# Kernel tuning notes

Hardware: AMD Instinct MI355X
Metric: run time of the kernel (lower is better)

The kernel has to match this reference:

```python
import jax, jax.numpy as jnp
import numpy as np

S, B, D, H, L = 512, 64, 1024, 1024, 2


def setup_inputs() -> dict:
    key = jax.random.key(0)
    ks = jax.random.split(key, 10)
    stdv = 1.0 / np.sqrt(H)
    u = lambda k, shp: jax.random.uniform(k, shp, jnp.float32, -stdv, stdv)
    return {
        "x": jax.random.normal(ks[0], (S, B, D), jnp.float32),
        "hx": jnp.zeros((L, B, H), jnp.float32),
        "w_ih_0": u(ks[1], (3 * H, D)),
        "w_hh_0": u(ks[2], (3 * H, H)),
        "b_ih_0": u(ks[3], (3 * H,)),
        "b_hh_0": u(ks[4], (3 * H,)),
        "w_ih_1": u(ks[5], (3 * H, H)),
        "w_hh_1": u(ks[6], (3 * H, H)),
        "b_ih_1": u(ks[7], (3 * H,)),
        "b_hh_1": u(ks[8], (3 * H,)),
    }


def _gru_layer(x, h0, w_ih, w_hh, b_ih, b_hh):
    # Input-to-hidden projection for the whole sequence in one GEMM (same math,
    # x_t does not depend on the recurrence).  (S,B,3H)
    x_lin = jnp.einsum('sbd,gd->sbg', x, w_ih) + b_ih

    def step(h, xl):
        x_r, x_z, x_n = jnp.split(xl, 3, axis=-1)
        h_lin = h @ w_hh.T + b_hh  # (B,3H)
        h_r, h_z, h_n = jnp.split(h_lin, 3, axis=-1)
        r = jax.nn.sigmoid(x_r + h_r)
        z = jax.nn.sigmoid(x_z + h_z)
        n = jnp.tanh(x_n + r * h_n)
        h_new = (1.0 - z) * n + z * h
        return h_new, h_new

    h_last, ys = jax.lax.scan(step, h0, x_lin)
    return ys, h_last


def reference(x, hx, w_ih_0, w_hh_0, b_ih_0, b_hh_0,
              w_ih_1, w_hh_1, b_ih_1, b_hh_1):
    out0, h_f0 = _gru_layer(x, hx[0], w_ih_0, w_hh_0, b_ih_0, b_hh_0)
    out1, h_f1 = _gru_layer(out0, hx[1], w_ih_1, w_hh_1, b_ih_1, b_hh_1)
    hidden = jnp.stack([h_f0, h_f1], axis=0)  # (L,B,H)
    return out1, hidden
```

## Files before the change

### kernel.cpp

```cpp
#include <hip/hip_runtime.h>
#include <stdint.h>


#define SLEN 512
#define HB   65536
#define G3   3072
#define XLSLOT (64 * 64 * 48)

typedef __attribute__((ext_vector_type(8))) short bf16x8;
typedef __attribute__((ext_vector_type(4))) float f32x4;
typedef __attribute__((ext_vector_type(8))) uint16_t u16x8;

__device__ __forceinline__ uint16_t f32_to_bf16(float f) {
  uint32_t u = __float_as_uint(f);
  uint32_t r = u + 0x7FFFu + ((u >> 16) & 1u);
  return (uint16_t)(r >> 16);
}
__device__ __forceinline__ float sigmoid_fast(float x) { return 1.0f / (1.0f + __expf(-x)); }
__device__ __forceinline__ float tanh_fast(float x) { return 1.0f - 2.0f / (1.0f + __expf(2.0f * x)); }
__device__ __forceinline__ void async_cp16(const void* g, void* l) {
  __builtin_amdgcn_global_load_lds((const __attribute__((address_space(1))) void*)g,
                                   (__attribute__((address_space(3))) void*)l, 16, 0, 0);
}
__device__ __forceinline__ void st_u16_llc(uint16_t* p, uint16_t v) {
  __hip_atomic_store(p, v, __ATOMIC_RELAXED, __HIP_MEMORY_SCOPE_AGENT);
}
__device__ __forceinline__ void st_f32_llc(float* p, float v) {
  __hip_atomic_store(p, v, __ATOMIC_RELAXED, __HIP_MEMORY_SCOPE_AGENT);
}
__device__ __forceinline__ void drain_vmem() {
  asm volatile("s_waitcnt vmcnt(0)" ::: "memory");
}
__device__ __forceinline__ int ld_flag(const int* p) {
  return __hip_atomic_load(p, __ATOMIC_RELAXED, __HIP_MEMORY_SCOPE_AGENT);
}
__device__ __forceinline__ void st_flag(int* p, int v) {
  __hip_atomic_store(p, v, __ATOMIC_RELAXED, __HIP_MEMORY_SCOPE_AGENT);
}


__global__ __launch_bounds__(256) void convert_x(const float* __restrict__ src,
                                                 uint16_t* __restrict__ dst) {
  size_t i = ((size_t)blockIdx.x * 256 + threadIdx.x) * 8;
  const float4* s = (const float4*)(src + i);
  float4 a = s[0], b = s[1];
  u16x8 v;
  v[0] = f32_to_bf16(a.x); v[1] = f32_to_bf16(a.y);
  v[2] = f32_to_bf16(a.z); v[3] = f32_to_bf16(a.w);
  v[4] = f32_to_bf16(b.x); v[5] = f32_to_bf16(b.y);
  v[6] = f32_to_bf16(b.z); v[7] = f32_to_bf16(b.w);
  *(u16x8*)(dst + i) = v;
}

__global__ __launch_bounds__(256) void pack_w(const float* __restrict__ src,
                                              uint16_t* __restrict__ dst) {
  int tid = blockIdx.x * 256 + threadIdx.x;
  int tile = tid >> 11, rem = tid & 2047, ks = rem >> 6, lane = rem & 63;
  int row = tile * 16 + (lane & 15);
  int k0 = ks * 32 + (lane >> 4) * 8;
  const float* s = src + (size_t)row * 1024 + k0;
  u16x8 v;
#pragma unroll
  for (int j = 0; j < 8; ++j) v[j] = f32_to_bf16(s[j]);
  *(u16x8*)(dst + (size_t)tid * 8) = v;
}

__global__ __launch_bounds__(256) void init_state(const float* __restrict__ hx,
                                                  uint16_t* __restrict__ h0b,
                                                  uint16_t* __restrict__ h1b,
                                                  int* __restrict__ flags) {
  int i = blockIdx.x * 256 + threadIdx.x;
  h0b[i] = f32_to_bf16(hx[i]);
  h1b[i] = f32_to_bf16(hx[HB + i]);
  if (blockIdx.x < 16) flags[blockIdx.x * 256 + threadIdx.x] = 0;
}

__device__ __forceinline__ void poll_wait(const int* p0, int t0,
                                          const int* pa, int ta,
                                          const int* pb, int tb, int lane) {
  const int BIG = 0x7fffffff;
  int v0 = (t0 > 0) ? ld_flag(p0) : BIG;
  int va = (ta > 0) ? ld_flag(pa + lane * 16) : BIG;
  int vb = (tb > 0) ? ld_flag(pb + lane * 16) : BIG;
  int it = 0;
  while (!__all((v0 >= t0) & (va >= ta) & (vb >= tb))) {
    __builtin_amdgcn_s_sleep(1);
    if (v0 < t0) v0 = ld_flag(p0);
    if (va < ta) va = ld_flag(pa + lane * 16);
    if (vb < tb) vb = ld_flag(pb + lane * 16);
    if (++it > (1 << 24)) break;
  }
}


__device__ __forceinline__ void load_a16_sc1(const uint16_t* p, bf16x8* a) {
  asm volatile(
      "global_load_dwordx4 %0, %16, off sc1\n\t"
      "global_load_dwordx4 %1, %16, off offset:64 sc1\n\t"
      "global_load_dwordx4 %2, %16, off offset:128 sc1\n\t"
      "global_load_dwordx4 %3, %16, off offset:192 sc1\n\t"
      "global_load_dwordx4 %4, %16, off offset:256 sc1\n\t"
      "global_load_dwordx4 %5, %16, off offset:320 sc1\n\t"
      "global_load_dwordx4 %6, %16, off offset:384 sc1\n\t"
      "global_load_dwordx4 %7, %16, off offset:448 sc1\n\t"
      "global_load_dwordx4 %8, %16, off offset:512 sc1\n\t"
      "global_load_dwordx4 %9, %16, off offset:576 sc1\n\t"
      "global_load_dwordx4 %10, %16, off offset:640 sc1\n\t"
      "global_load_dwordx4 %11, %16, off offset:704 sc1\n\t"
      "global_load_dwordx4 %12, %16, off offset:768 sc1\n\t"
      "global_load_dwordx4 %13, %16, off offset:832 sc1\n\t"
      "global_load_dwordx4 %14, %16, off offset:896 sc1\n\t"
      "global_load_dwordx4 %15, %16, off offset:960 sc1\n\t"
      "s_waitcnt vmcnt(0)"
      : "=&v"(a[0]), "=&v"(a[1]), "=&v"(a[2]), "=&v"(a[3]),
        "=&v"(a[4]), "=&v"(a[5]), "=&v"(a[6]), "=&v"(a[7]),
        "=&v"(a[8]), "=&v"(a[9]), "=&v"(a[10]), "=&v"(a[11]),
        "=&v"(a[12]), "=&v"(a[13]), "=&v"(a[14]), "=&v"(a[15])
      : "v"(p)
      : "memory");
}

__device__ __forceinline__ void load_a16_xl12_sc1(const uint16_t* p, const float* px,
                                                  bf16x8* a, float* x) {
  asm volatile(
      "global_load_dword %16, %29, off sc1\n\t"
      "global_load_dword %17, %29, off offset:64 sc1\n\t"
      "global_load_dword %18, %29, off offset:128 sc1\n\t"
      "global_load_dword %19, %29, off offset:192 sc1\n\t"
      "global_load_dword %20, %29, off offset:256 sc1\n\t"
      "global_load_dword %21, %29, off offset:320 sc1\n\t"
      "global_load_dword %22, %29, off offset:384 sc1\n\t"
      "global_load_dword %23, %29, off offset:448 sc1\n\t"
      "global_load_dword %24, %29, off offset:512 sc1\n\t"
      "global_load_dword %25, %29, off offset:576 sc1\n\t"
      "global_load_dword %26, %29, off offset:640 sc1\n\t"
      "global_load_dword %27, %29, off offset:704 sc1\n\t"
      "global_load_dwordx4 %0, %28, off sc1\n\t"
      "global_load_dwordx4 %1, %28, off offset:64 sc1\n\t"
      "global_load_dwordx4 %2, %28, off offset:128 sc1\n\t"
      "global_load_dwordx4 %3, %28, off offset:192 sc1\n\t"
      "global_load_dwordx4 %4, %28, off offset:256 sc1\n\t"
      "global_load_dwordx4 %5, %28, off offset:320 sc1\n\t"
      "global_load_dwordx4 %6, %28, off offset:384 sc1\n\t"
      "global_load_dwordx4 %7, %28, off offset:448 sc1\n\t"
      "global_load_dwordx4 %8, %28, off offset:512 sc1\n\t"
      "global_load_dwordx4 %9, %28, off offset:576 sc1\n\t"
      "global_load_dwordx4 %10, %28, off offset:640 sc1\n\t"
      "global_load_dwordx4 %11, %28, off offset:704 sc1\n\t"
      "global_load_dwordx4 %12, %28, off offset:768 sc1\n\t"
      "global_load_dwordx4 %13, %28, off offset:832 sc1\n\t"
      "global_load_dwordx4 %14, %28, off offset:896 sc1\n\t"
      "global_load_dwordx4 %15, %28, off offset:960 sc1\n\t"
      "s_waitcnt vmcnt(0)"
      : "=&v"(a[0]), "=&v"(a[1]), "=&v"(a[2]), "=&v"(a[3]),
        "=&v"(a[4]), "=&v"(a[5]), "=&v"(a[6]), "=&v"(a[7]),
        "=&v"(a[8]), "=&v"(a[9]), "=&v"(a[10]), "=&v"(a[11]),
        "=&v"(a[12]), "=&v"(a[13]), "=&v"(a[14]), "=&v"(a[15]),
        "=&v"(x[0]), "=&v"(x[1]), "=&v"(x[2]), "=&v"(x[3]),
        "=&v"(x[4]), "=&v"(x[5]), "=&v"(x[6]), "=&v"(x[7]),
        "=&v"(x[8]), "=&v"(x[9]), "=&v"(x[10]), "=&v"(x[11])
      : "v"(p), "v"(px)
      : "memory");
}


__device__ __forceinline__ void mfma16(const bf16x8* av, const uint16_t* bbase, int lane,
                                       f32x4& acc0, f32x4& acc1, f32x4& acc2) {
#pragma unroll
  for (int ks = 0; ks < 16; ++ks) {
    const uint16_t* bp = bbase + (size_t)(ks * 64 + lane) * 8;
    bf16x8 b0 = *(const bf16x8*)(bp);
    bf16x8 b1 = *(const bf16x8*)(bp + 16384);
    bf16x8 b2 = *(const bf16x8*)(bp + 32768);
    acc0 = __builtin_amdgcn_mfma_f32_16x16x32_bf16(av[ks], b0, acc0, 0, 0, 0);
    acc1 = __builtin_amdgcn_mfma_f32_16x16x32_bf16(av[ks], b1, acc1, 0, 0, 0);
    acc2 = __builtin_amdgcn_mfma_f32_16x16x32_bf16(av[ks], b2, acc2, 0, 0, 0);
  }
}

__global__ __launch_bounds__(256, 1) void gru_persist(
    const uint16_t* __restrict__ x_bf,
    const uint16_t* __restrict__ wih0, const uint16_t* __restrict__ whh0,
    const uint16_t* __restrict__ wih1, const uint16_t* __restrict__ whh1,
    const float* __restrict__ bih0, const float* __restrict__ bhh0,
    const float* __restrict__ bih1, const float* __restrict__ bhh1,
    const float* __restrict__ hx,
    float* __restrict__ xl0, float* __restrict__ xl1,
    uint16_t* __restrict__ o0r,
    uint16_t* __restrict__ h0b, uint16_t* __restrict__ h1b,
    int* __restrict__ flags,
    float* __restrict__ out) {
  __shared__ uint16_t blds[49152];

  const int task = blockIdx.x >> 6;
  const int slice = blockIdx.x & 63;
  const int tid = threadIdx.x;
  const int lane = tid & 63;
  const int wv = tid >> 6;
  const int r15 = lane & 15;
  const int q = lane >> 4;
  const int c = slice * 16 + r15;
  const int m = 16 * wv + 4 * q;

  int* done0 = flags;
  int* done1 = flags + 1024;
  int* done2 = flags + 2048;
  int* done3 = flags + 3072;
  int* mydone = (task == 0) ? done0 : (task == 1) ? done1 : (task == 2) ? done2 : done3;

  const uint16_t* Bw = (task == 0) ? wih0 : (task == 1) ? whh0 : (task == 2) ? wih1 : whh1;
  const float* bv = (task == 0) ? bih0 : (task == 1) ? bhh0 : (task == 2) ? bih1 : bhh1;
  const float br = bv[c], bz = bv[1024 + c], bn = bv[2048 + c];

  float hreg[4];
  if (task == 1 || task == 3) {
    const int layer = (task == 3);
#pragma unroll
    for (int rg = 0; rg < 4; ++rg)
      hreg[rg] = hx[(size_t)layer * HB + (size_t)(m + rg) * 1024 + c];
  }

#pragma unroll
  for (int i = 0; i < 24; ++i) {
    int s2 = i * 256 + tid;
    int g = s2 >> 11, rem = s2 & 2047, ks = rem >> 6, l = rem & 63;
    const uint16_t* gp = Bw + (size_t)(g * 64 + slice) * 16384 +
                         (size_t)ks * 512 + l * 8;
    async_cp16(gp, blds + (size_t)s2 * 8);
  }
  drain_vmem();
  __syncthreads();

  for (int t = 0; t < SLEN; ++t) {
    if (wv == 0) {
      if (task == 0) {
        poll_wait(done1 + slice * 16, t - 3, flags, 0, flags, 0, lane);
      } else if (task == 1) {
        poll_wait(done0 + slice * 16, t + 1,
                  done1, t,
                  done2, t - 3, lane);
      } else if (task == 2) {
        poll_wait(done3 + slice * 16, t - 3,
                  done1, t + 1,
                  flags, 0, lane);
      } else {
        poll_wait(done2 + slice * 16, t + 1,
                  done3, t,
                  flags, 0, lane);
      }
    }
    __syncthreads();

    f32x4 acc0 = {0.f, 0.f, 0.f, 0.f}, acc1 = acc0, acc2 = acc0;
    bf16x8 av[16];
    float xv[12];

    if (task == 1 || task == 3) {
      const uint16_t* hb = (task == 1) ? h0b : h1b;
      const float* xlr = (task == 1) ? xl0 : xl1;
      const uint16_t* ap = hb + (size_t)(t & 1) * HB + (size_t)(16 * wv + r15) * 1024 + q * 8;
      const float* xlp = xlr + (size_t)(t & 3) * XLSLOT + (size_t)(slice * 64 + m) * 48 + r15;

      load_a16_xl12_sc1(ap, xlp, av, xv);
      mfma16(av, blds, lane, acc0, acc1, acc2);
      load_a16_sc1(ap + 512, av);
      mfma16(av, blds + 8192, lane, acc0, acc1, acc2);

      uint16_t* hbw = ((task == 1) ? h0b : h1b) + (size_t)((t + 1) & 1) * HB;
      uint16_t* orow = o0r + (size_t)(t & 3) * HB;
#pragma unroll
      for (int rg = 0; rg < 4; ++rg) {
        int mm = m + rg;
        float r = sigmoid_fast(xv[rg * 3 + 0] + acc0[rg] + br);
        float z = sigmoid_fast(xv[rg * 3 + 1] + acc1[rg] + bz);
        float n = tanh_fast(xv[rg * 3 + 2] + r * (acc2[rg] + bn));
        float h = (1.0f - z) * n + z * hreg[rg];
        hreg[rg] = h;
        uint16_t hb16 = f32_to_bf16(h);
        st_u16_llc(hbw + (size_t)mm * 1024 + c, hb16);
        if (task == 1) st_u16_llc(orow + (size_t)mm * 1024 + c, hb16);
        else out[(size_t)t * HB + (size_t)mm * 1024 + c] = h;
      }
    } else {
      if (task == 0) {
        const uint16_t* ap = x_bf + (size_t)t * HB + (size_t)(16 * wv + r15) * 1024 + q * 8;
#pragma unroll
        for (int ks = 0; ks < 16; ++ks) av[ks] = *(const bf16x8*)(ap + ks * 32);
        mfma16(av, blds, lane, acc0, acc1, acc2);
#pragma unroll
        for (int ks = 0; ks < 16; ++ks) av[ks] = *(const bf16x8*)(ap + 512 + ks * 32);
        mfma16(av, blds + 8192, lane, acc0, acc1, acc2);
      } else {
        const uint16_t* ap = o0r + (size_t)(t & 3) * HB + (size_t)(16 * wv + r15) * 1024 + q * 8;
        load_a16_sc1(ap, av);
        mfma16(av, blds, lane, acc0, acc1, acc2);
        load_a16_sc1(ap + 512, av);
        mfma16(av, blds + 8192, lane, acc0, acc1, acc2);
      }
      float* dst = ((task == 0) ? xl0 : xl1) + (size_t)(t & 3) * XLSLOT + (size_t)slice * 64 * 48;
#pragma unroll
      for (int rg = 0; rg < 4; ++rg) {
        int mm = m + rg;
        st_f32_llc(dst + (size_t)mm * 48 + r15,      acc0[rg] + br);
        st_f32_llc(dst + (size_t)mm * 48 + 16 + r15, acc1[rg] + bz);
        st_f32_llc(dst + (size_t)mm * 48 + 32 + r15, acc2[rg] + bn);
      }
    }

    drain_vmem();
    __syncthreads();
    if (tid == 0) st_flag(mydone + slice * 16, t + 1);
  }

  if (task == 1 || task == 3) {
    const int layer = (task == 3);
#pragma unroll
    for (int rg = 0; rg < 4; ++rg)
      out[(size_t)SLEN * HB + (size_t)layer * HB + (size_t)(m + rg) * 1024 + c] = hreg[rg];
  }
}


extern "C" void kernel_launch(void* const* d_in, const int* in_sizes, int n_in,
                              void* d_out, int out_size, void* d_ws, size_t ws_size,
                              hipStream_t stream) {
  (void)in_sizes; (void)n_in; (void)out_size; (void)ws_size;
  const float* x = (const float*)d_in[0];
  const float* hx = (const float*)d_in[1];
  const float* wih0f = (const float*)d_in[2];
  const float* whh0f = (const float*)d_in[3];
  const float* bih0 = (const float*)d_in[4];
  const float* bhh0 = (const float*)d_in[5];
  const float* wih1f = (const float*)d_in[6];
  const float* whh1f = (const float*)d_in[7];
  const float* bih1 = (const float*)d_in[8];
  const float* bhh1 = (const float*)d_in[9];
  float* out = (float*)d_out;

  char* ws = (char*)d_ws;
  uint16_t* x_bf = (uint16_t*)ws; ws += (size_t)SLEN * HB * 2;
  uint16_t* wih0 = (uint16_t*)ws; ws += (size_t)G3 * 1024 * 2;
  uint16_t* whh0 = (uint16_t*)ws; ws += (size_t)G3 * 1024 * 2;
  uint16_t* wih1 = (uint16_t*)ws; ws += (size_t)G3 * 1024 * 2;
  uint16_t* whh1 = (uint16_t*)ws; ws += (size_t)G3 * 1024 * 2;
  float* xl0 = (float*)ws; ws += (size_t)4 * XLSLOT * 4;
  float* xl1 = (float*)ws; ws += (size_t)4 * XLSLOT * 4;
  uint16_t* o0r = (uint16_t*)ws; ws += (size_t)4 * HB * 2;
  uint16_t* h0b = (uint16_t*)ws; ws += (size_t)2 * HB * 2;
  uint16_t* h1b = (uint16_t*)ws; ws += (size_t)2 * HB * 2;
  int* flags = (int*)ws; ws += 16384;

  convert_x<<<16384, 256, 0, stream>>>(x, x_bf);
  pack_w<<<1536, 256, 0, stream>>>(wih0f, wih0);
  pack_w<<<1536, 256, 0, stream>>>(whh0f, whh0);
  pack_w<<<1536, 256, 0, stream>>>(wih1f, wih1);
  pack_w<<<1536, 256, 0, stream>>>(whh1f, whh1);
  init_state<<<256, 256, 0, stream>>>(hx, h0b, h1b, flags);

  const uint16_t* cx = x_bf;
  const uint16_t* cw0 = wih0; const uint16_t* cw1 = whh0;
  const uint16_t* cw2 = wih1; const uint16_t* cw3 = whh1;
  void* args[] = {(void*)&cx, (void*)&cw0, (void*)&cw1, (void*)&cw2, (void*)&cw3,
                  (void*)&bih0, (void*)&bhh0, (void*)&bih1, (void*)&bhh1, (void*)&hx,
                  (void*)&xl0, (void*)&xl1, (void*)&o0r, (void*)&h0b, (void*)&h1b,
                  (void*)&flags, (void*)&out};
  hipError_t e = hipLaunchCooperativeKernel(reinterpret_cast<void*>(gru_persist),
                                            dim3(256), dim3(256), args, 0u, stream);
  if (e != hipSuccess) {
    gru_persist<<<dim3(256), dim3(256), 0, stream>>>(
        x_bf, wih0, whh0, wih1, whh1, bih0, bhh0, bih1, bhh1, hx,
        xl0, xl1, o0r, h0b, h1b, flags, out);
  }
}
```

Before: 4.262 ms.

## Use per-wave completion flags with vector polling and overlap second A-load with MFMA

Each wave now publishes its own done flag (slice*16+wv) instead of a block-wide barrier followed by a single thread store, and pollers read four per-wave flags with one dwordx4 load and take the minimum. The second half of the A operand is issued before the first MFMA batch so its load latency overlaps with compute, using a separate register array. This removes one __syncthreads per step and hides load latency, at the cost of more VGPRs and more polled flag traffic. The timeout limit on polling is also lowered.

```diff
diff --git a/kernel.cpp b/kernel.cpp
--- a/kernel.cpp
+++ b/kernel.cpp
@@ -10,6 +10,7 @@
 typedef __attribute__((ext_vector_type(8))) short bf16x8;
 typedef __attribute__((ext_vector_type(4))) float f32x4;
 typedef __attribute__((ext_vector_type(8))) uint16_t u16x8;
+typedef __attribute__((ext_vector_type(4))) int i32x4;
 
 __device__ __forceinline__ uint16_t f32_to_bf16(float f) {
   uint32_t u = __float_as_uint(f);
@@ -31,11 +32,19 @@
 __device__ __forceinline__ void drain_vmem() {
   asm volatile("s_waitcnt vmcnt(0)" ::: "memory");
 }
-__device__ __forceinline__ int ld_flag(const int* p) {
-  return __hip_atomic_load(p, __ATOMIC_RELAXED, __HIP_MEMORY_SCOPE_AGENT);
-}
 __device__ __forceinline__ void st_flag(int* p, int v) {
   __hip_atomic_store(p, v, __ATOMIC_RELAXED, __HIP_MEMORY_SCOPE_AGENT);
+}
+__device__ __forceinline__ i32x4 ld_flag4(const int* p) {
+  i32x4 r;
+  asm volatile("global_load_dwordx4 %0, %1, off sc1\n\ts_waitcnt vmcnt(0)"
+               : "=v"(r) : "v"(p) : "memory");
+  return r;
+}
+__device__ __forceinline__ int min4(i32x4 v) {
+  int a = v[0] < v[1] ? v[0] : v[1];
+  int b = v[2] < v[3] ? v[2] : v[3];
+  return a < b ? a : b;
 }
 
 
@@ -75,20 +84,20 @@
   if (blockIdx.x < 16) flags[blockIdx.x * 256 + threadIdx.x] = 0;
 }
 
-__device__ __forceinline__ void poll_wait(const int* p0, int t0,
-                                          const int* pa, int ta,
-                                          const int* pb, int tb, int lane) {
+__device__ __forceinline__ void poll3(const int* pa, int ta,
+                                      const int* pb, int tb,
+                                      const int* pc, int tc) {
   const int BIG = 0x7fffffff;
-  int v0 = (t0 > 0) ? ld_flag(p0) : BIG;
-  int va = (ta > 0) ? ld_flag(pa + lane * 16) : BIG;
-  int vb = (tb > 0) ? ld_flag(pb + lane * 16) : BIG;
+  int va = (ta > 0) ? min4(ld_flag4(pa)) : BIG;
+  int vb = (tb > 0) ? min4(ld_flag4(pb)) : BIG;
+  int vc = (tc > 0) ? min4(ld_flag4(pc)) : BIG;
   int it = 0;
-  while (!__all((v0 >= t0) & (va >= ta) & (vb >= tb))) {
+  while (!__all((va >= ta) & (vb >= tb) & (vc >= tc))) {
     __builtin_amdgcn_s_sleep(1);
-    if (v0 < t0) v0 = ld_flag(p0);
-    if (va < ta) va = ld_flag(pa + lane * 16);
-    if (vb < tb) vb = ld_flag(pb + lane * 16);
-    if (++it > (1 << 24)) break;
+    if (va < ta) va = min4(ld_flag4(pa));
+    if (vb < tb) vb = min4(ld_flag4(pb));
+    if (vc < tc) vc = min4(ld_flag4(pc));
+    if (++it > (1 << 22)) break;
   }
 }
 
@@ -112,6 +121,32 @@
       "global_load_dwordx4 %14, %16, off offset:896 sc1\n\t"
       "global_load_dwordx4 %15, %16, off offset:960 sc1\n\t"
       "s_waitcnt vmcnt(0)"
+      : "=&v"(a[0]), "=&v"(a[1]), "=&v"(a[2]), "=&v"(a[3]),
+        "=&v"(a[4]), "=&v"(a[5]), "=&v"(a[6]), "=&v"(a[7]),
+        "=&v"(a[8]), "=&v"(a[9]), "=&v"(a[10]), "=&v"(a[11]),
+        "=&v"(a[12]), "=&v"(a[13]), "=&v"(a[14]), "=&v"(a[15])
+      : "v"(p)
+      : "memory");
+}
+
+__device__ __forceinline__ void issue_a16_sc1(const uint16_t* p, bf16x8* a) {
+  asm volatile(
+      "global_load_dwordx4 %0, %16, off sc1\n\t"
+      "global_load_dwordx4 %1, %16, off offset:64 sc1\n\t"
+      "global_load_dwordx4 %2, %16, off offset:128 sc1\n\t"
+      "global_load_dwordx4 %3, %16, off offset:192 sc1\n\t"
+      "global_load_dwordx4 %4, %16, off offset:256 sc1\n\t"
+      "global_load_dwordx4 %5, %16, off offset:320 sc1\n\t"
+      "global_load_dwordx4 %6, %16, off offset:384 sc1\n\t"
+      "global_load_dwordx4 %7, %16, off offset:448 sc1\n\t"
+      "global_load_dwordx4 %8, %16, off offset:512 sc1\n\t"
+      "global_load_dwordx4 %9, %16, off offset:576 sc1\n\t"
+      "global_load_dwordx4 %10, %16, off offset:640 sc1\n\t"
+      "global_load_dwordx4 %11, %16, off offset:704 sc1\n\t"
+      "global_load_dwordx4 %12, %16, off offset:768 sc1\n\t"
+      "global_load_dwordx4 %13, %16, off offset:832 sc1\n\t"
+      "global_load_dwordx4 %14, %16, off offset:896 sc1\n\t"
+      "global_load_dwordx4 %15, %16, off offset:960 sc1"
       : "=&v"(a[0]), "=&v"(a[1]), "=&v"(a[2]), "=&v"(a[3]),
         "=&v"(a[4]), "=&v"(a[5]), "=&v"(a[6]), "=&v"(a[7]),
         "=&v"(a[8]), "=&v"(a[9]), "=&v"(a[10]), "=&v"(a[11]),
@@ -207,6 +242,7 @@
   int* done2 = flags + 2048;
   int* done3 = flags + 3072;
   int* mydone = (task == 0) ? done0 : (task == 1) ? done1 : (task == 2) ? done2 : done3;
+  int* myflag = mydone + slice * 16 + wv;
 
   const uint16_t* Bw = (task == 0) ? wih0 : (task == 1) ? whh0 : (task == 2) ? wih1 : whh1;
   const float* bv = (task == 0) ? bih0 : (task == 1) ? bhh0 : (task == 2) ? bih1 : bhh1;
@@ -234,25 +270,26 @@
   for (int t = 0; t < SLEN; ++t) {
     if (wv == 0) {
       if (task == 0) {
-        poll_wait(done1 + slice * 16, t - 3, flags, 0, flags, 0, lane);
+        poll3(done1 + slice * 16, t - 3,
+              flags, 0, flags, 0);
       } else if (task == 1) {
-        poll_wait(done0 + slice * 16, t + 1,
-                  done1, t,
-                  done2, t - 3, lane);
+        poll3(done0 + slice * 16, t + 1,
+              done1 + lane * 16, t,
+              done2 + lane * 16, t - 3);
       } else if (task == 2) {
-        poll_wait(done3 + slice * 16, t - 3,
-                  done1, t + 1,
-                  flags, 0, lane);
+        poll3(done1 + lane * 16, t + 1,
+              done3 + slice * 16, t - 3,
+              flags, 0);
       } else {
-        poll_wait(done2 + slice * 16, t + 1,
-                  done3, t,
-                  flags, 0, lane);
+        poll3(done2 + slice * 16, t + 1,
+              done3 + lane * 16, t,
+              flags, 0);
       }
     }
     __syncthreads();
 
     f32x4 acc0 = {0.f, 0.f, 0.f, 0.f}, acc1 = acc0, acc2 = acc0;
-    bf16x8 av[16];
+    bf16x8 av0[16], av1[16];
     float xv[12];
 
     if (task == 1 || task == 3) {
@@ -261,10 +298,12 @@
       const uint16_t* ap = hb + (size_t)(t & 1) * HB + (size_t)(16 * wv + r15) * 1024 + q * 8;
       const float* xlp = xlr + (size_t)(t & 3) * XLSLOT + (size_t)(slice * 64 + m) * 48 + r15;
 
-      load_a16_xl12_sc1(ap, xlp, av, xv);
-      mfma16(av, blds, lane, acc0, acc1, acc2);
-      load_a16_sc1(ap + 512, av);
-      mfma16(av, blds + 8192, lane, acc0, acc1, acc2);
+      load_a16_xl12_sc1(ap, xlp, av0, xv);
+      issue_a16_sc1(ap + 512, av1);
+      mfma16(av0, blds, lane, acc0, acc1, acc2);
+      asm volatile("s_waitcnt vmcnt(0)" ::: "memory");
+      __builtin_amdgcn_sched_barrier(0);
+      mfma16(av1, blds + 8192, lane, acc0, acc1, acc2);
 
       uint16_t* hbw = ((task == 1) ? h0b : h1b) + (size_t)((t + 1) & 1) * HB;
       uint16_t* orow = o0r + (size_t)(t & 3) * HB;
@@ -285,17 +324,19 @@
       if (task == 0) {
         const uint16_t* ap = x_bf + (size_t)t * HB + (size_t)(16 * wv + r15) * 1024 + q * 8;
 #pragma unroll
-        for (int ks = 0; ks < 16; ++ks) av[ks] = *(const bf16x8*)(ap + ks * 32);
-        mfma16(av, blds, lane, acc0, acc1, acc2);
-#pragma unroll
-        for (int ks = 0; ks < 16; ++ks) av[ks] = *(const bf16x8*)(ap + 512 + ks * 32);
-        mfma16(av, blds + 8192, lane, acc0, acc1, acc2);
+        for (int ks = 0; ks < 16; ++ks) av0[ks] = *(const bf16x8*)(ap + ks * 32);
+#pragma unroll
+        for (int ks = 0; ks < 16; ++ks) av1[ks] = *(const bf16x8*)(ap + 512 + ks * 32);
+        mfma16(av0, blds, lane, acc0, acc1, acc2);
+        mfma16(av1, blds + 8192, lane, acc0, acc1, acc2);
       } else {
         const uint16_t* ap = o0r + (size_t)(t & 3) * HB + (size_t)(16 * wv + r15) * 1024 + q * 8;
-        load_a16_sc1(ap, av);
-        mfma16(av, blds, lane, acc0, acc1, acc2);
-        load_a16_sc1(ap + 512, av);
-        mfma16(av, blds + 8192, lane, acc0, acc1, acc2);
+        load_a16_sc1(ap, av0);
+        issue_a16_sc1(ap + 512, av1);
+        mfma16(av0, blds, lane, acc0, acc1, acc2);
+        asm volatile("s_waitcnt vmcnt(0)" ::: "memory");
+        __builtin_amdgcn_sched_barrier(0);
+        mfma16(av1, blds + 8192, lane, acc0, acc1, acc2);
       }
       float* dst = ((task == 0) ? xl0 : xl1) + (size_t)(t & 3) * XLSLOT + (size_t)slice * 64 * 48;
 #pragma unroll
@@ -308,8 +349,7 @@
     }
 
     drain_vmem();
-    __syncthreads();
-    if (tid == 0) st_flag(mydone + slice * 16, t + 1);
+    st_flag(myflag, t + 1);
   }
 
   if (task == 1 || task == 3) {
```

Result: slower. 4.818 ms (+13.0%).

## Split per-step dependency waits by K-half and deepen ring buffers to eight

Applied to the files above, without the earlier changes.

The per-step wait is split so each block first waits only on the producers of the first half of the K dimension, runs those MFMAs, then waits on the second-half producers before continuing. The done flag is now published before the layer-1 output store, and the xl/o0r ring buffers grow from four to eight slots so producers can run further ahead. The aim is to shorten the critical path of the recurrent chain by overlapping compute with the slower producers. The cost is an extra barrier and polling round per step, plus a shorter spin-timeout bound.

```diff
diff --git a/kernel.cpp b/kernel.cpp
--- a/kernel.cpp
+++ b/kernel.cpp
@@ -75,20 +75,20 @@
   if (blockIdx.x < 16) flags[blockIdx.x * 256 + threadIdx.x] = 0;
 }
 
-__device__ __forceinline__ void poll_wait(const int* p0, int t0,
-                                          const int* pa, int ta,
-                                          const int* pb, int tb, int lane) {
+__device__ __forceinline__ void pollA(const int* a0, int t0,
+                                      const int* a1, int t1,
+                                      const int* a2, int t2) {
   const int BIG = 0x7fffffff;
-  int v0 = (t0 > 0) ? ld_flag(p0) : BIG;
-  int va = (ta > 0) ? ld_flag(pa + lane * 16) : BIG;
-  int vb = (tb > 0) ? ld_flag(pb + lane * 16) : BIG;
+  int v0 = (t0 > 0) ? ld_flag(a0) : BIG;
+  int v1 = (t1 > 0) ? ld_flag(a1) : BIG;
+  int v2 = (t2 > 0) ? ld_flag(a2) : BIG;
   int it = 0;
-  while (!__all((v0 >= t0) & (va >= ta) & (vb >= tb))) {
+  while (!__all((v0 >= t0) & (v1 >= t1) & (v2 >= t2))) {
     __builtin_amdgcn_s_sleep(1);
-    if (v0 < t0) v0 = ld_flag(p0);
-    if (va < ta) va = ld_flag(pa + lane * 16);
-    if (vb < tb) vb = ld_flag(pb + lane * 16);
-    if (++it > (1 << 24)) break;
+    if (v0 < t0) v0 = ld_flag(a0);
+    if (v1 < t1) v1 = ld_flag(a1);
+    if (v2 < t2) v2 = ld_flag(a2);
+    if (++it > (1 << 22)) break;
   }
 }
 
@@ -231,22 +231,31 @@
   drain_vmem();
   __syncthreads();
 
+  const int* pw_d1 = done1 + lane * 16;
+  const int* pw_d2 = done2 + lane * 16;
+  const int* pw_d3 = done3 + lane * 16;
+  const int* sl_d0 = done0 + slice * 16;
+  const int* sl_d1 = done1 + slice * 16;
+  const int* sl_d2 = done2 + slice * 16;
+  const int* sl_d3 = done3 + slice * 16;
+  const int lo = (lane < 32);
+
   for (int t = 0; t < SLEN; ++t) {
     if (wv == 0) {
       if (task == 0) {
-        poll_wait(done1 + slice * 16, t - 3, flags, 0, flags, 0, lane);
+        pollA(sl_d1, t - 7, flags, 0, flags, 0);
       } else if (task == 1) {
-        poll_wait(done0 + slice * 16, t + 1,
-                  done1, t,
-                  done2, t - 3, lane);
+        pollA(sl_d0, t + 1,
+              pw_d1, lo ? t : 0,
+              pw_d2, t - 7);
       } else if (task == 2) {
-        poll_wait(done3 + slice * 16, t - 3,
-                  done1, t + 1,
-                  flags, 0, lane);
+        pollA(sl_d3, t - 7,
+              pw_d1, lo ? t + 1 : 0,
+              flags, 0);
       } else {
-        poll_wait(done2 + slice * 16, t + 1,
-                  done3, t,
-                  flags, 0, lane);
+        pollA(sl_d2, t + 1,
+              pw_d3, lo ? t : 0,
+              flags, 0);
       }
     }
     __syncthreads();
@@ -259,15 +268,19 @@
       const uint16_t* hb = (task == 1) ? h0b : h1b;
       const float* xlr = (task == 1) ? xl0 : xl1;
       const uint16_t* ap = hb + (size_t)(t & 1) * HB + (size_t)(16 * wv + r15) * 1024 + q * 8;
-      const float* xlp = xlr + (size_t)(t & 3) * XLSLOT + (size_t)(slice * 64 + m) * 48 + r15;
+      const float* xlp = xlr + (size_t)(t & 7) * XLSLOT + (size_t)(slice * 64 + m) * 48 + r15;
 
       load_a16_xl12_sc1(ap, xlp, av, xv);
       mfma16(av, blds, lane, acc0, acc1, acc2);
+
+      if (wv == 0) pollA(pw_d1 + ((task == 3) ? 2048 : 0), lo ? 0 : t, flags, 0, flags, 0);
+      __syncthreads();
+
       load_a16_sc1(ap + 512, av);
       mfma16(av, blds + 8192, lane, acc0, acc1, acc2);
 
       uint16_t* hbw = ((task == 1) ? h0b : h1b) + (size_t)((t + 1) & 1) * HB;
-      uint16_t* orow = o0r + (size_t)(t & 3) * HB;
+      uint16_t* orow = o0r + (size_t)(t & 7) * HB;
 #pragma unroll
       for (int rg = 0; rg < 4; ++rg) {
         int mm = m + rg;
@@ -279,7 +292,14 @@
         uint16_t hb16 = f32_to_bf16(h);
         st_u16_llc(hbw + (size_t)mm * 1024 + c, hb16);
         if (task == 1) st_u16_llc(orow + (size_t)mm * 1024 + c, hb16);
-        else out[(size_t)t * HB + (size_t)mm * 1024 + c] = h;
+      }
+      drain_vmem();
+      __syncthreads();
+      if (tid == 0) st_flag(mydone + slice * 16, t + 1);
+      if (task == 3) {
+#pragma unroll
+        for (int rg = 0; rg < 4; ++rg)
+          out[(size_t)t * HB + (size_t)(m + rg) * 1024 + c] = hreg[rg];
       }
     } else {
       if (task == 0) {
@@ -291,13 +311,17 @@
         for (int ks = 0; ks < 16; ++ks) av[ks] = *(const bf16x8*)(ap + 512 + ks * 32);
         mfma16(av, blds + 8192, lane, acc0, acc1, acc2);
       } else {
-        const uint16_t* ap = o0r + (size_t)(t & 3) * HB + (size_t)(16 * wv + r15) * 1024 + q * 8;
+        const uint16_t* ap = o0r + (size_t)(t & 7) * HB + (size_t)(16 * wv + r15) * 1024 + q * 8;
         load_a16_sc1(ap, av);
         mfma16(av, blds, lane, acc0, acc1, acc2);
+
+        if (wv == 0) pollA(pw_d1, lo ? 0 : t + 1, flags, 0, flags, 0);
+        __syncthreads();
+
         load_a16_sc1(ap + 512, av);
         mfma16(av, blds + 8192, lane, acc0, acc1, acc2);
       }
-      float* dst = ((task == 0) ? xl0 : xl1) + (size_t)(t & 3) * XLSLOT + (size_t)slice * 64 * 48;
+      float* dst = ((task == 0) ? xl0 : xl1) + (size_t)(t & 7) * XLSLOT + (size_t)slice * 64 * 48;
 #pragma unroll
       for (int rg = 0; rg < 4; ++rg) {
         int mm = m + rg;
@@ -305,11 +329,10 @@
         st_f32_llc(dst + (size_t)mm * 48 + 16 + r15, acc1[rg] + bz);
         st_f32_llc(dst + (size_t)mm * 48 + 32 + r15, acc2[rg] + bn);
       }
+      drain_vmem();
+      __syncthreads();
+      if (tid == 0) st_flag(mydone + slice * 16, t + 1);
     }
-
-    drain_vmem();
-    __syncthreads();
-    if (tid == 0) st_flag(mydone + slice * 16, t + 1);
   }
 
   if (task == 1 || task == 3) {
@@ -343,9 +366,9 @@
   uint16_t* whh0 = (uint16_t*)ws; ws += (size_t)G3 * 1024 * 2;
   uint16_t* wih1 = (uint16_t*)ws; ws += (size_t)G3 * 1024 * 2;
   uint16_t* whh1 = (uint16_t*)ws; ws += (size_t)G3 * 1024 * 2;
-  float* xl0 = (float*)ws; ws += (size_t)4 * XLSLOT * 4;
-  float* xl1 = (float*)ws; ws += (size_t)4 * XLSLOT * 4;
-  uint16_t* o0r = (uint16_t*)ws; ws += (size_t)4 * HB * 2;
+  float* xl0 = (float*)ws; ws += (size_t)8 * XLSLOT * 4;
+  float* xl1 = (float*)ws; ws += (size_t)8 * XLSLOT * 4;
+  uint16_t* o0r = (uint16_t*)ws; ws += (size_t)8 * HB * 2;
   uint16_t* h0b = (uint16_t*)ws; ws += (size_t)2 * HB * 2;
   uint16_t* h1b = (uint16_t*)ws; ws += (size_t)2 * HB * 2;
   int* flags = (int*)ws; ws += 16384;
```

Result: slower. 4.468 ms (+4.8%).
